# Kernel tuning notes

Hardware: AMD Instinct MI355X
Metric: run time of the kernel (lower is better)

Reference implementation:

```python
import jax, jax.numpy as jnp
import numpy as np

N_HEADS = 16
EMBED = 1024
SEQ = 2048
BATCH = 4
GELU_C = 0.044715
EPS = 1e-5


def gelu_tanh(x):
    return 0.5 * x * (1.0 + jnp.tanh(jnp.sqrt(2.0 / jnp.pi) * (x + GELU_C * x ** 3)))


def layer_norm(x, scale, shift):
    mean = jnp.mean(x, axis=-1, keepdims=True)
    var = jnp.var(x, axis=-1, keepdims=True)
    return scale * (x - mean) / jnp.sqrt(var + EPS) + shift


def setup_inputs() -> dict:
    key = jax.random.key(0)
    ks = jax.random.split(key, 8)
    d = EMBED
    s = 0.02
    return {
        "X": jax.random.normal(ks[0], (BATCH, SEQ, d), dtype=jnp.float32),
        "Wq": jax.random.normal(ks[1], (d, d), dtype=jnp.float32) * s,
        "Wk": jax.random.normal(ks[2], (d, d), dtype=jnp.float32) * s,
        "Wv": jax.random.normal(ks[3], (d, d), dtype=jnp.float32) * s,
        "Wo": jax.random.normal(ks[4], (d, d), dtype=jnp.float32) * s,
        "W1": jax.random.normal(ks[5], (d, 4 * d), dtype=jnp.float32) * s,
        "b1": jnp.zeros((4 * d,), dtype=jnp.float32),
        "W2": jax.random.normal(ks[6], (4 * d, d), dtype=jnp.float32) * s,
        "b2": jnp.zeros((d,), dtype=jnp.float32),
        "ln1_scale": jnp.ones((d,), dtype=jnp.float32),
        "ln1_shift": jnp.zeros((d,), dtype=jnp.float32),
        "ln2_scale": jnp.ones((d,), dtype=jnp.float32),
        "ln2_shift": jnp.zeros((d,), dtype=jnp.float32),
    }


def attention(x, Wq, Wk, Wv, Wo):
    b, s, d = x.shape
    h, dh = N_HEADS, d // N_HEADS
    q = (x @ Wq).reshape(b, s, h, dh).transpose(0, 2, 1, 3)  # [b,h,s,dh]
    k = (x @ Wk).reshape(b, s, h, dh).transpose(0, 2, 1, 3)
    v = (x @ Wv).reshape(b, s, h, dh).transpose(0, 2, 1, 3)
    scores = jnp.einsum("bhqd,bhkd->bhqk", q, k) / jnp.sqrt(jnp.float32(dh))
    causal = jnp.tril(jnp.ones((s, s), dtype=bool))
    scores = jnp.where(causal, scores, -jnp.inf)
    w = jax.nn.softmax(scores, axis=-1)  # dropout rate 0 -> identity
    ctx = jnp.einsum("bhqk,bhkd->bhqd", w, v)
    ctx = ctx.transpose(0, 2, 1, 3).reshape(b, s, d)
    return ctx @ Wo


def reference(X, Wq, Wk, Wv, Wo, W1, b1, W2, b2,
              ln1_scale, ln1_shift, ln2_scale, ln2_shift):
    h = layer_norm(X, ln1_scale, ln1_shift)
    X = X + attention(h, Wq, Wk, Wv, Wo)
    h = layer_norm(X, ln2_scale, ln2_shift)
    h = gelu_tanh(h @ W1 + b1) @ W2 + b2
    return X + h
```

## Files before the change

### kernel.cpp

```cpp
#include <hip/hip_runtime.h>

typedef unsigned short u16;
typedef __attribute__((ext_vector_type(8))) short bf16x8;
typedef __attribute__((ext_vector_type(4))) float fx4;

#define MFMA16(a, b, c) __builtin_amdgcn_mfma_f32_16x16x32_bf16((a), (b), (c), 0, 0, 0)

__device__ __forceinline__ u16 f2bf(float f) {
  unsigned u = __float_as_uint(f);
  u += 0x7fffu + ((u >> 16) & 1u);
  return (u16)(u >> 16);
}

__device__ __forceinline__ void gload_lds16(const void* g, void* l) {
  __builtin_amdgcn_global_load_lds((const __attribute__((address_space(1))) void*)g,
                                   (__attribute__((address_space(3))) void*)l,
                                   16, 0, 0);
}

struct WP {
  const float* s[6];
  u16* d[6];
};
__global__ __launch_bounds__(256) void tcvt_all(WP p) {
  __shared__ float t[32][33];
  const int id = blockIdx.x;
  int which, bx, by, R, C;
  if (id < 4096) {
    which = id >> 10;
    const int q = id & 1023;
    bx = q >> 5; by = q & 31; R = 1024; C = 1024;
  } else if (id < 8192) {
    which = 4;
    const int q = id - 4096;
    bx = q & 127; by = q >> 7; R = 1024; C = 4096;
  } else {
    which = 5;
    const int q = id - 8192;
    bx = q & 31; by = q >> 5; R = 4096; C = 1024;
  }
  const float* src = p.s[which];
  u16* dst = p.d[which];
  const int tx = threadIdx.x & 31, ty = threadIdx.x >> 5;
#pragma unroll
  for (int i = 0; i < 4; ++i)
    t[ty + i * 8][tx] = src[(size_t)(by * 32 + ty + i * 8) * C + bx * 32 + tx];
  __syncthreads();
#pragma unroll
  for (int i = 0; i < 4; ++i)
    dst[(size_t)(bx * 32 + ty + i * 8) * R + by * 32 + tx] = f2bf(t[tx][ty + i * 8]);
}

__global__ __launch_bounds__(256) void ln_kernel(const float* __restrict__ x,
                                                 const float* __restrict__ sc,
                                                 const float* __restrict__ sh,
                                                 u16* __restrict__ out) {
  const int row = blockIdx.x, tid = threadIdx.x;
  const float4 v = ((const float4*)(x + (size_t)row * 1024))[tid];
  float s = v.x + v.y + v.z + v.w;
  float ss = v.x * v.x + v.y * v.y + v.z * v.z + v.w * v.w;
#pragma unroll
  for (int d = 32; d >= 1; d >>= 1) {
    s += __shfl_xor(s, d);
    ss += __shfl_xor(ss, d);
  }
  __shared__ float rs[4], rq[4];
  const int w = tid >> 6;
  if ((tid & 63) == 0) { rs[w] = s; rq[w] = ss; }
  __syncthreads();
  s = rs[0] + rs[1] + rs[2] + rs[3];
  ss = rq[0] + rq[1] + rq[2] + rq[3];
  const float mean = s * (1.f / 1024.f);
  const float var = ss * (1.f / 1024.f) - mean * mean;
  const float rstd = rsqrtf(var + 1e-5f);
  const float4 g = ((const float4*)sc)[tid];
  const float4 b = ((const float4*)sh)[tid];
  ushort4 o;
  o.x = f2bf(g.x * (v.x - mean) * rstd + b.x);
  o.y = f2bf(g.y * (v.y - mean) * rstd + b.y);
  o.z = f2bf(g.z * (v.z - mean) * rstd + b.z);
  o.w = f2bf(g.w * (v.w - mean) * rstd + b.w);
  ((ushort4*)(out + (size_t)row * 1024))[tid] = o;
}

__device__ __forceinline__ void xcd_map(int bid, int NTN, int& tMi, int& tNi) {
  const int xcd = bid & 7, i = bid >> 3;
  tMi = xcd + 8 * (i / NTN);
  tNi = i % NTN;
}

#define EPILOGUE(MODE, MRv)                                                        \
  _Pragma("unroll") for (int m = 0; m < (MRv); ++m) {                              \
    const int rgb = tM + wm * ((MRv) * 16) + m * 16 + hi * 4;                      \
    _Pragma("unroll") for (int n = 0; n < 4; ++n) {                                \
      const int cg = tN + wn * 64 + n * 16 + lo;                                   \
      _Pragma("unroll") for (int r = 0; r < 4; ++r) {                              \
        const float v = acc[m][n][r];                                              \
        const int rg = rgb + r;                                                    \
        if constexpr ((MODE) == 0) {                                               \
          const int which = cg >> 10, c = cg & 1023;                               \
          const int head = c >> 6, dhi = c & 63;                                   \
          const int b = rg >> 11, sidx = rg & 2047;                                \
          const int bh = b * 16 + head;                                            \
          const u16 bv = f2bf(v);                                                  \
          if (which == 0)      qd[((size_t)bh * 2048 + sidx) * 64 + dhi] = bv;     \
          else if (which == 1) kd[((size_t)bh * 2048 + sidx) * 64 + dhi] = bv;     \
          else                 vd[((size_t)bh * 64 + dhi) * 2048 + sidx] = bv;     \
        } else if constexpr ((MODE) == 1) {                                        \
          float* o = (float*)outp;                                                 \
          const size_t idx = (size_t)rg * 1024 + cg;                               \
          o[idx] = aux[idx] + v;                                                   \
        } else if constexpr ((MODE) == 2) {                                        \
          const float xx = v + aux[cg];                                            \
          const float t2 = xx + 0.044715f * xx * xx * xx;                          \
          const float e = __expf(1.5957691216057308f * t2);                        \
          const float th = 1.f - 2.f / (e + 1.f);                                  \
          ((u16*)outp)[(size_t)rg * 4096 + cg] = f2bf(0.5f * xx * (1.f + th));     \
        } else {                                                                   \
          float* o = (float*)outp;                                                 \
          const size_t idx = (size_t)rg * 1024 + cg;                               \
          o[idx] = o[idx] + v + aux[cg];                                           \
        }                                                                          \
      }                                                                            \
    }                                                                              \
  }

template <int MODE>
__global__ __launch_bounds__(512, 1) void gemm4p(
    const u16* __restrict__ A, const u16* __restrict__ Bt, int K, int NTN,
    void* __restrict__ outp, const float* __restrict__ aux,
    u16* __restrict__ qd, u16* __restrict__ kd, u16* __restrict__ vd) {
  __shared__ u16 lA[2][2][256 * 32];
  __shared__ u16 lB[2][2][128 * 32];
  const int tid = threadIdx.x;
  const int lane = tid & 63, w = tid >> 6;
  const int lo = lane & 15, hi = lane >> 4;
  const int wm = w >> 1, wn = w & 1;
  int tMi, tNi;
  xcd_map(blockIdx.x, NTN, tMi, tNi);
  const int tM = tMi * 256, tN = tNi * 128;
  const int NT = K >> 6;
  const int NIT = K >> 7;

#define STG4(TI, H, GK)                                                           \
  do {                                                                            \
    _Pragma("unroll") for (int j = 0; j < 2; ++j) {                               \
      const int idx = j * 512 + tid;                                              \
      const int row = idx >> 2, u = idx & 3;                                      \
      gload_lds16(A + (size_t)(tM + row) * K + (GK) + ((u ^ ((row >> 1) & 3)) * 8), \
                  &lA[TI][H][idx * 8]);                                           \
    }                                                                             \
    {                                                                             \
      const int row = tid >> 2, u = tid & 3;                                      \
      gload_lds16(Bt + (size_t)(tN + row) * K + (GK) + ((u ^ ((row >> 1) & 3)) * 8), \
                  &lB[TI][H][tid * 8]);                                           \
    }                                                                             \
  } while (0)

#define PHASE4(TI, H, STAGE_STMT, VMSTR)                                          \
  {                                                                               \
    bf16x8 afr[4], bfr[4];                                                        \
    _Pragma("unroll") for (int mi = 0; mi < 4; ++mi) {                            \
      const int R = wm * 64 + mi * 16 + lo;                                       \
      afr[mi] = *(const bf16x8*)&lA[TI][H][R * 32 + ((hi ^ ((R >> 1) & 3)) * 8)]; \
    }                                                                             \
    _Pragma("unroll") for (int n = 0; n < 4; ++n) {                               \
      const int R = wn * 64 + n * 16 + lo;                                        \
      bfr[n] = *(const bf16x8*)&lB[TI][H][R * 32 + ((hi ^ ((R >> 1) & 3)) * 8)];  \
    }                                                                             \
    STAGE_STMT;                                                                   \
    asm volatile("s_waitcnt " VMSTR ::: "memory");                                \
    __builtin_amdgcn_s_barrier();                                                 \
    asm volatile("s_waitcnt lgkmcnt(0)" ::: "memory");                            \
    __builtin_amdgcn_sched_barrier(0);                                            \
    __builtin_amdgcn_s_setprio(1);                                                \
    _Pragma("unroll") for (int mi = 0; mi < 4; ++mi)                              \
      _Pragma("unroll") for (int n = 0; n < 4; ++n)                               \
        acc[mi][n] = MFMA16(afr[mi], bfr[n], acc[mi][n]);                         \
    __builtin_amdgcn_s_setprio(0);                                                \
    __builtin_amdgcn_sched_barrier(0);                                            \
    __builtin_amdgcn_s_barrier();                                                 \
    __builtin_amdgcn_sched_barrier(0);                                            \
  }

  fx4 acc[4][4];
#pragma unroll
  for (int m = 0; m < 4; ++m)
#pragma unroll
    for (int n = 0; n < 4; ++n) acc[m][n] = (fx4){0.f, 0.f, 0.f, 0.f};

  STG4(0, 0, 0);
  STG4(0, 1, 32);
  STG4(1, 0, 64);
  asm volatile("s_waitcnt vmcnt(6)" ::: "memory");
  __builtin_amdgcn_s_barrier();
  __builtin_amdgcn_sched_barrier(0);

  for (int it = 0; it < NIT - 1; ++it) {
    const int t0 = 2 * it;
    PHASE4(0, 0, STG4(1, 1, (t0 + 1) * 64 + 32), "vmcnt(6)")
    PHASE4(0, 1, STG4(0, 0, (t0 + 2) * 64), "vmcnt(6)")
    PHASE4(1, 0, STG4(0, 1, (t0 + 2) * 64 + 32), "vmcnt(6)")
    PHASE4(1, 1, STG4(1, 0, (t0 + 3) * 64), "vmcnt(6)")
  }
  {
    const int t0 = NT - 2;
    PHASE4(0, 0, STG4(1, 1, (t0 + 1) * 64 + 32), "vmcnt(6)")
    PHASE4(0, 1, ((void)0), "vmcnt(3)")
    PHASE4(1, 0, ((void)0), "vmcnt(0)")
    PHASE4(1, 1, ((void)0), "vmcnt(0)")
  }
#undef PHASE4
#undef STG4

  EPILOGUE(MODE, 4)
}

template <int MODE>
__global__ __launch_bounds__(512, 1) void gemm8p(
    const u16* __restrict__ A, const u16* __restrict__ Bt, int K, int NTN,
    void* __restrict__ outp, const float* __restrict__ aux,
    u16* __restrict__ qd, u16* __restrict__ kd, u16* __restrict__ vd) {
  constexpr int MR = 8, MR2 = 4;
  __shared__ u16 lA[2][2][256 * 32];
  __shared__ u16 lB[2][2][256 * 32];
  const int tid = threadIdx.x;
  const int lane = tid & 63, w = tid >> 6;
  const int lo = lane & 15, hi = lane >> 4;
  const int wm = w >> 2, wn = w & 3;
  int tMi, tNi;
  xcd_map(blockIdx.x, NTN, tMi, tNi);
  const int tM = tMi * 256, tN = tNi * 256;
  const int NT = K >> 6;
  const int NIT = K >> 7;

#define STG_A(TI, KSH, GK)                                                        \
  do {                                                                            \
    _Pragma("unroll") for (int j = 0; j < 2; ++j) {                               \
      const int idx = j * 512 + tid;                                              \
      const int row = idx >> 2, u = idx & 3;                                      \
      gload_lds16(A + (size_t)(tM + row) * K + (GK) + ((u ^ ((row >> 1) & 3)) * 8), \
                  &lA[TI][KSH][idx * 8]);                                         \
    }                                                                             \
  } while (0)
#define STG_B(TI, KSH, GK)                                                        \
  do {                                                                            \
    _Pragma("unroll") for (int j = 0; j < 2; ++j) {                               \
      const int idx = j * 512 + tid;                                              \
      const int row = idx >> 2, u = idx & 3;                                      \
      gload_lds16(Bt + (size_t)(tN + row) * K + (GK) + ((u ^ ((row >> 1) & 3)) * 8), \
                  &lB[TI][KSH][idx * 8]);                                         \
    }                                                                             \
  } while (0)
#define VMW asm volatile("s_waitcnt vmcnt(4)" ::: "memory")
#define NOPS ((void)0)

#define PHASE(P, STAGE_STMT, VM)                                                  \
  {                                                                               \
    constexpr int ksg = (P) >> 1;                                                 \
    constexpr int mh = (P) & 1;                                                   \
    constexpr int ti = ksg >> 1;                                                  \
    constexpr int ksh = ksg & 1;                                                  \
    bf16x8 afr[MR2];                                                              \
    _Pragma("unroll") for (int mi = 0; mi < MR2; ++mi) {                          \
      const int R = wm * (MR * 16) + (mh * MR2 + mi) * 16 + lo;                   \
      afr[mi] =                                                                   \
          *(const bf16x8*)&lA[ti][ksh][R * 32 + ((hi ^ ((R >> 1) & 3)) * 8)];     \
    }                                                                             \
    if constexpr (mh == 0) {                                                      \
      _Pragma("unroll") for (int n = 0; n < 4; ++n) {                             \
        const int R = wn * 64 + n * 16 + lo;                                      \
        bfr[n] =                                                                  \
            *(const bf16x8*)&lB[ti][ksh][R * 32 + ((hi ^ ((R >> 1) & 3)) * 8)];   \
      }                                                                           \
    }                                                                             \
    STAGE_STMT;                                                                   \
    VM;                                                                           \
    __builtin_amdgcn_s_barrier();                                                 \
    asm volatile("s_waitcnt lgkmcnt(0)" ::: "memory");                            \
    __builtin_amdgcn_sched_barrier(0);                                            \
    __builtin_amdgcn_s_setprio(1);                                                \
    _Pragma("unroll") for (int mi = 0; mi < MR2; ++mi)                            \
      _Pragma("unroll") for (int n = 0; n < 4; ++n)                               \
        acc[mh * MR2 + mi][n] = MFMA16(afr[mi], bfr[n], acc[mh * MR2 + mi][n]);   \
    __builtin_amdgcn_s_setprio(0);                                                \
    __builtin_amdgcn_sched_barrier(0);                                            \
    __builtin_amdgcn_s_barrier();                                                 \
    __builtin_amdgcn_sched_barrier(0);                                            \
  }

  fx4 acc[MR][4];
#pragma unroll
  for (int m = 0; m < MR; ++m)
#pragma unroll
    for (int n = 0; n < 4; ++n) acc[m][n] = (fx4){0.f, 0.f, 0.f, 0.f};
  bf16x8 bfr[4];

  STG_A(0, 0, 0);
  STG_B(0, 0, 0);
  STG_A(0, 1, 32);
  STG_B(0, 1, 32);
  STG_A(1, 0, 64);
  STG_B(1, 0, 64);
  asm volatile("s_waitcnt vmcnt(4)" ::: "memory");
  __builtin_amdgcn_s_barrier();
  __builtin_amdgcn_sched_barrier(0);

  for (int it = 0; it < NIT; ++it) {
    const int t0 = 2 * it;
    const bool g2 = (t0 + 2) < NT, g3 = (t0 + 3) < NT;
    PHASE(0, STG_A(1, 1, (t0 + 1) * 64 + 32), NOPS)
    PHASE(1, STG_B(1, 1, (t0 + 1) * 64 + 32), NOPS)
    PHASE(2, if (g2) STG_A(0, 0, (t0 + 2) * 64), NOPS)
    PHASE(3, if (g2) STG_B(0, 0, (t0 + 2) * 64), VMW)
    PHASE(4, if (g2) STG_A(0, 1, (t0 + 2) * 64 + 32), NOPS)
    PHASE(5, if (g2) STG_B(0, 1, (t0 + 2) * 64 + 32), NOPS)
    PHASE(6, if (g3) STG_A(1, 0, (t0 + 3) * 64), NOPS)
    PHASE(7, if (g3) STG_B(1, 0, (t0 + 3) * 64), VMW)
  }
#undef PHASE
#undef STG_A
#undef STG_B
#undef VMW
#undef NOPS

  EPILOGUE(MODE, MR)
}

__global__ __launch_bounds__(512) void attn_kernel(const u16* __restrict__ Q,
                                                   const u16* __restrict__ Kg,
                                                   const u16* __restrict__ Vt,
                                                   u16* __restrict__ ctx) {
  __shared__ u16 lK[2][64 * 64];
  __shared__ u16 lV[2][64 * 64];
  __shared__ u16 Plds[8][16 * 64];
  const int tid = threadIdx.x;
  const int w = tid >> 6, lane = tid & 63;
  const int lo = lane & 15, hi = lane >> 4;
  const int bh = blockIdx.x;
  const int j = blockIdx.y;
  const u16* Qb = Q + (size_t)bh * 2048 * 64;
  const u16* Kb = Kg + (size_t)bh * 2048 * 64;
  const u16* Vb = Vt + (size_t)bh * 64 * 2048;
  u16* Pw = Plds[w];
  const int nt0 = 2 * j + 2;

  const int rowS = tid >> 3;
  const int ugS = (tid & 7) ^ (rowS & 7);

#define STAGE(BUF, KB)                                                         \
  do {                                                                         \
    gload_lds16(Kb + (size_t)((KB) + rowS) * 64 + ugS * 8, &lK[BUF][tid * 8]); \
    gload_lds16(Vb + (size_t)rowS * 2048 + (KB) + ugS * 8, &lV[BUF][tid * 8]); \
  } while (0)

  const int b = bh >> 4, h = bh & 15;
  const float SCALE = 0.18033688011112042f;

  bf16x8 ones;
#pragma unroll
  for (int i = 0; i < 8; ++i) ones[i] = (short)0x3F80;

  int qt = j;
  int qw = qt * 128 + w * 16;

  bf16x8 qf[2];
#pragma unroll
  for (int kc = 0; kc < 2; ++kc)
    qf[kc] = *(const bf16x8*)&Qb[(size_t)(qw + lo) * 64 + kc * 32 + hi * 8];

  fx4 accO[4];
  fx4 accS = (fx4){0.f, 0.f, 0.f, 0.f};
#pragma unroll
  for (int t2 = 0; t2 < 4; ++t2) accO[t2] = (fx4){0.f, 0.f, 0.f, 0.f};

  STAGE(0, 0);
  __syncthreads();

  int buf = 0;
  for (int t = 0; t < 34; ++t) {
    if (t + 1 < 34) {
      const int tn = t + 1;
      const int kbn = (tn < nt0 ? tn : tn - nt0) * 64;
      STAGE(buf ^ 1, kbn);
    }
    if (t == nt0) {
#pragma unroll
      for (int t2 = 0; t2 < 4; ++t2)
#pragma unroll
        for (int r = 0; r < 4; ++r) {
          const int rg = b * 2048 + qw + hi * 4 + r;
          const int cg = h * 64 + t2 * 16 + lo;
          ctx[(size_t)rg * 1024 + cg] = f2bf(accO[t2][r] / accS[r]);
        }
      qt = 15 - j;
      qw = qt * 128 + w * 16;
#pragma unroll
      for (int kc = 0; kc < 2; ++kc)
        qf[kc] = *(const bf16x8*)&Qb[(size_t)(qw + lo) * 64 + kc * 32 + hi * 8];
#pragma unroll
      for (int t2 = 0; t2 < 4; ++t2) accO[t2] = (fx4){0.f, 0.f, 0.f, 0.f};
      accS = (fx4){0.f, 0.f, 0.f, 0.f};
    }
    const int kb = (t < nt0 ? t : t - nt0) * 64;
    if (kb <= qw + 15) {
      const u16* lKb = lK[buf];
      const u16* lVb = lV[buf];
      fx4 s[4];
#pragma unroll
      for (int tt = 0; tt < 4; ++tt) {
        const int r = tt * 16 + lo;
        const bf16x8 kf0 = *(const bf16x8*)&lKb[r * 64 + ((hi ^ (r & 7)) << 3)];
        const bf16x8 kf1 = *(const bf16x8*)&lKb[r * 64 + (((4 + hi) ^ (r & 7)) << 3)];
        fx4 z = (fx4){0.f, 0.f, 0.f, 0.f};
        z = MFMA16(qf[0], kf0, z);
        z = MFMA16(qf[1], kf1, z);
        s[tt] = z;
      }
      if (kb + 63 > qw) {
#pragma unroll
        for (int tt = 0; tt < 4; ++tt)
#pragma unroll
          for (int r = 0; r < 4; ++r) {
            const int key = kb + tt * 16 + lo;
            const int qr = qw + hi * 4 + r;
            s[tt][r] = (key > qr) ? 0.f : exp2f(s[tt][r] * SCALE);
          }
      } else {
#pragma unroll
        for (int tt = 0; tt < 4; ++tt)
#pragma unroll
          for (int r = 0; r < 4; ++r) s[tt][r] = exp2f(s[tt][r] * SCALE);
      }
#pragma unroll
      for (int r = 0; r < 4; ++r) {
        unsigned pk01, pk23;
        asm("v_cvt_pk_bf16_f32 %0, %1, %2" : "=v"(pk01) : "v"(s[0][r]), "v"(s[1][r]));
        asm("v_cvt_pk_bf16_f32 %0, %1, %2" : "=v"(pk23) : "v"(s[2][r]), "v"(s[3][r]));
        const int row = hi * 4 + r;
        const int sw = (row & 7) << 4;
        const int rbase = row * 128;
        Pw[(rbase + (((0 * 16 + lo) * 2) ^ sw)) >> 1] = (u16)pk01;
        Pw[(rbase + (((1 * 16 + lo) * 2) ^ sw)) >> 1] = (u16)(pk01 >> 16);
        Pw[(rbase + (((2 * 16 + lo) * 2) ^ sw)) >> 1] = (u16)pk23;
        Pw[(rbase + (((3 * 16 + lo) * 2) ^ sw)) >> 1] = (u16)(pk23 >> 16);
      }
      asm volatile("s_waitcnt lgkmcnt(0)" ::: "memory");
      bf16x8 pf[2];
#pragma unroll
      for (int kc = 0; kc < 2; ++kc) {
        const int row = lo;
        const int colB = kc * 64 + hi * 16;
        pf[kc] = *(const bf16x8*)((const char*)Pw + row * 128 + (colB ^ ((row & 7) << 4)));
      }
      accS = MFMA16(pf[0], ones, accS);
      accS = MFMA16(pf[1], ones, accS);
#pragma unroll
      for (int t2 = 0; t2 < 4; ++t2) {
        const int r2 = t2 * 16 + lo;
        const bf16x8 vf0 = *(const bf16x8*)&lVb[r2 * 64 + ((hi ^ (r2 & 7)) << 3)];
        const bf16x8 vf1 = *(const bf16x8*)&lVb[r2 * 64 + (((4 + hi) ^ (r2 & 7)) << 3)];
        accO[t2] = MFMA16(pf[0], vf0, accO[t2]);
        accO[t2] = MFMA16(pf[1], vf1, accO[t2]);
      }
    }
    __syncthreads();
    buf ^= 1;
  }
#pragma unroll
  for (int t2 = 0; t2 < 4; ++t2)
#pragma unroll
    for (int r = 0; r < 4; ++r) {
      const int rg = b * 2048 + qw + hi * 4 + r;
      const int cg = h * 64 + t2 * 16 + lo;
      ctx[(size_t)rg * 1024 + cg] = f2bf(accO[t2][r] / accS[r]);
    }
#undef STAGE
}

extern "C" void kernel_launch(void* const* d_in, const int* in_sizes, int n_in,
                              void* d_out, int out_size, void* d_ws, size_t ws_size,
                              hipStream_t stream) {
  const float* X    = (const float*)d_in[0];
  const float* Wq   = (const float*)d_in[1];
  const float* Wk   = (const float*)d_in[2];
  const float* Wv   = (const float*)d_in[3];
  const float* Wo   = (const float*)d_in[4];
  const float* W1   = (const float*)d_in[5];
  const float* b1   = (const float*)d_in[6];
  const float* W2   = (const float*)d_in[7];
  const float* b2   = (const float*)d_in[8];
  const float* ln1s = (const float*)d_in[9];
  const float* ln1b = (const float*)d_in[10];
  const float* ln2s = (const float*)d_in[11];
  const float* ln2b = (const float*)d_in[12];

  const size_t SZ_WQKVT = 3072UL * 1024;
  const size_t SZ_WOT   = 1024UL * 1024;
  const size_t SZ_W1T   = 4096UL * 1024;
  const size_t SZ_W2T   = 1024UL * 4096;
  const size_t SZ_H     = 8192UL * 1024;
  const size_t SZ_QKV   = 64UL * 2048 * 64;

  u16* WqkvT = (u16*)d_ws;
  u16* WoT   = WqkvT + SZ_WQKVT;
  u16* W1T   = WoT + SZ_WOT;
  u16* W2T   = W1T + SZ_W1T;
  u16* hbuf  = W2T + SZ_W2T;
  u16* qbuf  = hbuf + SZ_H;
  u16* kbuf  = qbuf + SZ_QKV;
  u16* vbuf  = kbuf + SZ_QKV;
  u16* gbuf  = vbuf + SZ_QKV;
  u16* ctx   = hbuf;
  u16* h2    = qbuf;

  float* out = (float*)d_out;
  dim3 blk(256);

  WP wp;
  wp.s[0] = Wq; wp.s[1] = Wk; wp.s[2] = Wv; wp.s[3] = Wo; wp.s[4] = W1; wp.s[5] = W2;
  wp.d[0] = WqkvT;
  wp.d[1] = WqkvT + 1024 * 1024;
  wp.d[2] = WqkvT + 2 * 1024 * 1024;
  wp.d[3] = WoT;
  wp.d[4] = W1T;
  wp.d[5] = W2T;
  tcvt_all<<<12288, blk, 0, stream>>>(wp);

  ln_kernel<<<8192, blk, 0, stream>>>(X, ln1s, ln1b, hbuf);
  gemm4p<0><<<768, dim3(512), 0, stream>>>(hbuf, WqkvT, 1024, 24,
                                           nullptr, nullptr, qbuf, kbuf, vbuf);
  attn_kernel<<<dim3(64, 8), dim3(512), 0, stream>>>(qbuf, kbuf, vbuf, ctx);
  gemm4p<1><<<256, dim3(512), 0, stream>>>(ctx, WoT, 1024, 8,
                                           out, X, nullptr, nullptr, nullptr);
  ln_kernel<<<8192, blk, 0, stream>>>(out, ln2s, ln2b, h2);
  gemm8p<2><<<512, dim3(512), 0, stream>>>(h2, W1T, 1024, 16,
                                           gbuf, b1, nullptr, nullptr, nullptr);
  gemm4p<3><<<256, dim3(512), 0, stream>>>(gbuf, W2T, 4096, 8,
                                           out, b2, nullptr, nullptr, nullptr);
}
```

Measured before the change: 396.5 us.

## Double-buffer LDS fragment registers to overlap ds_reads with MFMAs in GEMMs

Both GEMM kernels (gemm4p-style and gemm8p) now hold two register sets for the A and B fragments. The LDS reads for the next phase are issued right after the barrier, alongside the current phase's MFMA block, instead of before it. The goal is to hide LDS read latency behind matrix math. This costs more VGPRs, and the lgkmcnt(0) wait at the next phase may still stall. In gemm8p the mid-loop vmcnt waits also change from every fourth phase to every phase, and the loop gains a peeled tail.

```diff
diff --git a/kernel.cpp b/kernel.cpp
--- a/kernel.cpp
+++ b/kernel.cpp
@@ -157,26 +157,30 @@
     }                                                                             \
   } while (0)
 
-#define PHASE4(TI, H, STAGE_STMT, VMSTR)                                          \
-  {                                                                               \
-    bf16x8 afr[4], bfr[4];                                                        \
+#define LDFRAG4(AF, BF, TI, H)                                                    \
+  do {                                                                            \
     _Pragma("unroll") for (int mi = 0; mi < 4; ++mi) {                            \
       const int R = wm * 64 + mi * 16 + lo;                                       \
-      afr[mi] = *(const bf16x8*)&lA[TI][H][R * 32 + ((hi ^ ((R >> 1) & 3)) * 8)]; \
+      AF[mi] = *(const bf16x8*)&lA[TI][H][R * 32 + ((hi ^ ((R >> 1) & 3)) * 8)];  \
     }                                                                             \
     _Pragma("unroll") for (int n = 0; n < 4; ++n) {                               \
       const int R = wn * 64 + n * 16 + lo;                                        \
-      bfr[n] = *(const bf16x8*)&lB[TI][H][R * 32 + ((hi ^ ((R >> 1) & 3)) * 8)];  \
-    }                                                                             \
+      BF[n] = *(const bf16x8*)&lB[TI][H][R * 32 + ((hi ^ ((R >> 1) & 3)) * 8)];   \
+    }                                                                             \
+  } while (0)
+
+#define PHASE4(CA, CB, PREF_STMT, STAGE_STMT, VMSTR)                              \
+  {                                                                               \
     STAGE_STMT;                                                                   \
     asm volatile("s_waitcnt " VMSTR ::: "memory");                                \
     __builtin_amdgcn_s_barrier();                                                 \
     asm volatile("s_waitcnt lgkmcnt(0)" ::: "memory");                            \
     __builtin_amdgcn_sched_barrier(0);                                            \
+    PREF_STMT;                                                                    \
     __builtin_amdgcn_s_setprio(1);                                                \
     _Pragma("unroll") for (int mi = 0; mi < 4; ++mi)                              \
       _Pragma("unroll") for (int n = 0; n < 4; ++n)                               \
-        acc[mi][n] = MFMA16(afr[mi], bfr[n], acc[mi][n]);                         \
+        acc[mi][n] = MFMA16(CA[mi], CB[n], acc[mi][n]);                           \
     __builtin_amdgcn_s_setprio(0);                                                \
     __builtin_amdgcn_sched_barrier(0);                                            \
     __builtin_amdgcn_s_barrier();                                                 \
@@ -188,6 +192,7 @@
   for (int m = 0; m < 4; ++m)
 #pragma unroll
     for (int n = 0; n < 4; ++n) acc[m][n] = (fx4){0.f, 0.f, 0.f, 0.f};
+  bf16x8 afrA[4], bfrA[4], afrB[4], bfrB[4];
 
   STG4(0, 0, 0);
   STG4(0, 1, 32);
@@ -195,22 +200,24 @@
   asm volatile("s_waitcnt vmcnt(6)" ::: "memory");
   __builtin_amdgcn_s_barrier();
   __builtin_amdgcn_sched_barrier(0);
+  LDFRAG4(afrA, bfrA, 0, 0);
 
   for (int it = 0; it < NIT - 1; ++it) {
     const int t0 = 2 * it;
-    PHASE4(0, 0, STG4(1, 1, (t0 + 1) * 64 + 32), "vmcnt(6)")
-    PHASE4(0, 1, STG4(0, 0, (t0 + 2) * 64), "vmcnt(6)")
-    PHASE4(1, 0, STG4(0, 1, (t0 + 2) * 64 + 32), "vmcnt(6)")
-    PHASE4(1, 1, STG4(1, 0, (t0 + 3) * 64), "vmcnt(6)")
+    PHASE4(afrA, bfrA, LDFRAG4(afrB, bfrB, 0, 1), STG4(1, 1, (t0 + 1) * 64 + 32), "vmcnt(6)")
+    PHASE4(afrB, bfrB, LDFRAG4(afrA, bfrA, 1, 0), STG4(0, 0, (t0 + 2) * 64), "vmcnt(6)")
+    PHASE4(afrA, bfrA, LDFRAG4(afrB, bfrB, 1, 1), STG4(0, 1, (t0 + 2) * 64 + 32), "vmcnt(6)")
+    PHASE4(afrB, bfrB, LDFRAG4(afrA, bfrA, 0, 0), STG4(1, 0, (t0 + 3) * 64), "vmcnt(6)")
   }
   {
     const int t0 = NT - 2;
-    PHASE4(0, 0, STG4(1, 1, (t0 + 1) * 64 + 32), "vmcnt(6)")
-    PHASE4(0, 1, ((void)0), "vmcnt(3)")
-    PHASE4(1, 0, ((void)0), "vmcnt(0)")
-    PHASE4(1, 1, ((void)0), "vmcnt(0)")
+    PHASE4(afrA, bfrA, LDFRAG4(afrB, bfrB, 0, 1), STG4(1, 1, (t0 + 1) * 64 + 32), "vmcnt(6)")
+    PHASE4(afrB, bfrB, LDFRAG4(afrA, bfrA, 1, 0), ((void)0), "vmcnt(3)")
+    PHASE4(afrA, bfrA, LDFRAG4(afrB, bfrB, 1, 1), ((void)0), "vmcnt(0)")
+    PHASE4(afrB, bfrB, ((void)0), ((void)0), "vmcnt(0)")
   }
 #undef PHASE4
+#undef LDFRAG4
 #undef STG4
 
   EPILOGUE(MODE, 4)
@@ -221,7 +228,6 @@
     const u16* __restrict__ A, const u16* __restrict__ Bt, int K, int NTN,
     void* __restrict__ outp, const float* __restrict__ aux,
     u16* __restrict__ qd, u16* __restrict__ kd, u16* __restrict__ vd) {
-  constexpr int MR = 8, MR2 = 4;
   __shared__ u16 lA[2][2][256 * 32];
   __shared__ u16 lB[2][2][256 * 32];
   const int tid = threadIdx.x;
@@ -231,7 +237,6 @@
   int tMi, tNi;
   xcd_map(blockIdx.x, NTN, tMi, tNi);
   const int tM = tMi * 256, tN = tNi * 256;
-  const int NT = K >> 6;
   const int NIT = K >> 7;
 
 #define STG_A(TI, KSH, GK)                                                        \
@@ -252,49 +257,46 @@
                   &lB[TI][KSH][idx * 8]);                                         \
     }                                                                             \
   } while (0)
-#define VMW asm volatile("s_waitcnt vmcnt(4)" ::: "memory")
-#define NOPS ((void)0)
-
-#define PHASE(P, STAGE_STMT, VM)                                                  \
+
+#define LDA8(AF, TI, KSH, MH)                                                     \
+  do {                                                                            \
+    _Pragma("unroll") for (int mi = 0; mi < 4; ++mi) {                            \
+      const int R = wm * 128 + ((MH) * 4 + mi) * 16 + lo;                         \
+      AF[mi] = *(const bf16x8*)&lA[TI][KSH][R * 32 + ((hi ^ ((R >> 1) & 3)) * 8)]; \
+    }                                                                             \
+  } while (0)
+#define LDB8(BF, TI, KSH)                                                         \
+  do {                                                                            \
+    _Pragma("unroll") for (int n = 0; n < 4; ++n) {                               \
+      const int R = wn * 64 + n * 16 + lo;                                        \
+      BF[n] = *(const bf16x8*)&lB[TI][KSH][R * 32 + ((hi ^ ((R >> 1) & 3)) * 8)]; \
+    }                                                                             \
+  } while (0)
+
+#define PHASE8(MH, CA, CB, PREF_STMT, STAGE_STMT, VMSTR)                          \
   {                                                                               \
-    constexpr int ksg = (P) >> 1;                                                 \
-    constexpr int mh = (P) & 1;                                                   \
-    constexpr int ti = ksg >> 1;                                                  \
-    constexpr int ksh = ksg & 1;                                                  \
-    bf16x8 afr[MR2];                                                              \
-    _Pragma("unroll") for (int mi = 0; mi < MR2; ++mi) {                          \
-      const int R = wm * (MR * 16) + (mh * MR2 + mi) * 16 + lo;                   \
-      afr[mi] =                                                                   \
-          *(const bf16x8*)&lA[ti][ksh][R * 32 + ((hi ^ ((R >> 1) & 3)) * 8)];     \
-    }                                                                             \
-    if constexpr (mh == 0) {                                                      \
-      _Pragma("unroll") for (int n = 0; n < 4; ++n) {                             \
-        const int R = wn * 64 + n * 16 + lo;                                      \
-        bfr[n] =                                                                  \
-            *(const bf16x8*)&lB[ti][ksh][R * 32 + ((hi ^ ((R >> 1) & 3)) * 8)];   \
-      }                                                                           \
-    }                                                                             \
     STAGE_STMT;                                                                   \
-    VM;                                                                           \
+    asm volatile("s_waitcnt " VMSTR ::: "memory");                                \
     __builtin_amdgcn_s_barrier();                                                 \
     asm volatile("s_waitcnt lgkmcnt(0)" ::: "memory");                            \
     __builtin_amdgcn_sched_barrier(0);                                            \
+    PREF_STMT;                                                                    \
     __builtin_amdgcn_s_setprio(1);                                                \
-    _Pragma("unroll") for (int mi = 0; mi < MR2; ++mi)                            \
+    _Pragma("unroll") for (int mi = 0; mi < 4; ++mi)                              \
       _Pragma("unroll") for (int n = 0; n < 4; ++n)                               \
-        acc[mh * MR2 + mi][n] = MFMA16(afr[mi], bfr[n], acc[mh * MR2 + mi][n]);   \
+        acc[(MH) * 4 + mi][n] = MFMA16(CA[mi], CB[n], acc[(MH) * 4 + mi][n]);     \
     __builtin_amdgcn_s_setprio(0);                                                \
     __builtin_amdgcn_sched_barrier(0);                                            \
     __builtin_amdgcn_s_barrier();                                                 \
     __builtin_amdgcn_sched_barrier(0);                                            \
   }
 
-  fx4 acc[MR][4];
-#pragma unroll
-  for (int m = 0; m < MR; ++m)
+  fx4 acc[8][4];
+#pragma unroll
+  for (int m = 0; m < 8; ++m)
 #pragma unroll
     for (int n = 0; n < 4; ++n) acc[m][n] = (fx4){0.f, 0.f, 0.f, 0.f};
-  bf16x8 bfr[4];
+  bf16x8 afrA[4], afrB[4], bfrA[4], bfrB[4];
 
   STG_A(0, 0, 0);
   STG_B(0, 0, 0);
@@ -305,26 +307,38 @@
   asm volatile("s_waitcnt vmcnt(4)" ::: "memory");
   __builtin_amdgcn_s_barrier();
   __builtin_amdgcn_sched_barrier(0);
-
-  for (int it = 0; it < NIT; ++it) {
+  LDA8(afrA, 0, 0, 0);
+  LDB8(bfrA, 0, 0);
+
+  for (int it = 0; it < NIT - 1; ++it) {
     const int t0 = 2 * it;
-    const bool g2 = (t0 + 2) < NT, g3 = (t0 + 3) < NT;
-    PHASE(0, STG_A(1, 1, (t0 + 1) * 64 + 32), NOPS)
-    PHASE(1, STG_B(1, 1, (t0 + 1) * 64 + 32), NOPS)
-    PHASE(2, if (g2) STG_A(0, 0, (t0 + 2) * 64), NOPS)
-    PHASE(3, if (g2) STG_B(0, 0, (t0 + 2) * 64), VMW)
-    PHASE(4, if (g2) STG_A(0, 1, (t0 + 2) * 64 + 32), NOPS)
-    PHASE(5, if (g2) STG_B(0, 1, (t0 + 2) * 64 + 32), NOPS)
-    PHASE(6, if (g3) STG_A(1, 0, (t0 + 3) * 64), NOPS)
-    PHASE(7, if (g3) STG_B(1, 0, (t0 + 3) * 64), VMW)
-  }
-#undef PHASE
+    PHASE8(0, afrA, bfrA, LDA8(afrB, 0, 0, 1), STG_A(1, 1, (t0 + 1) * 64 + 32), "vmcnt(4)")
+    PHASE8(1, afrB, bfrA, { LDA8(afrA, 0, 1, 0); LDB8(bfrB, 0, 1); }, STG_B(1, 1, (t0 + 1) * 64 + 32), "vmcnt(4)")
+    PHASE8(0, afrA, bfrB, LDA8(afrB, 0, 1, 1), STG_A(0, 0, (t0 + 2) * 64), "vmcnt(4)")
+    PHASE8(1, afrB, bfrB, { LDA8(afrA, 1, 0, 0); LDB8(bfrA, 1, 0); }, STG_B(0, 0, (t0 + 2) * 64), "vmcnt(4)")
+    PHASE8(0, afrA, bfrA, LDA8(afrB, 1, 0, 1), STG_A(0, 1, (t0 + 2) * 64 + 32), "vmcnt(4)")
+    PHASE8(1, afrB, bfrA, { LDA8(afrA, 1, 1, 0); LDB8(bfrB, 1, 1); }, STG_B(0, 1, (t0 + 2) * 64 + 32), "vmcnt(4)")
+    PHASE8(0, afrA, bfrB, LDA8(afrB, 1, 1, 1), STG_A(1, 0, (t0 + 3) * 64), "vmcnt(4)")
+    PHASE8(1, afrB, bfrB, { LDA8(afrA, 0, 0, 0); LDB8(bfrA, 0, 0); }, STG_B(1, 0, (t0 + 3) * 64), "vmcnt(4)")
+  }
+  {
+    const int t0 = 2 * (NIT - 1);
+    PHASE8(0, afrA, bfrA, LDA8(afrB, 0, 0, 1), STG_A(1, 1, (t0 + 1) * 64 + 32), "vmcnt(4)")
+    PHASE8(1, afrB, bfrA, { LDA8(afrA, 0, 1, 0); LDB8(bfrB, 0, 1); }, STG_B(1, 1, (t0 + 1) * 64 + 32), "vmcnt(4)")
+    PHASE8(0, afrA, bfrB, LDA8(afrB, 0, 1, 1), ((void)0), "vmcnt(4)")
+    PHASE8(1, afrB, bfrB, { LDA8(afrA, 1, 0, 0); LDB8(bfrA, 1, 0); }, ((void)0), "vmcnt(4)")
+    PHASE8(0, afrA, bfrA, LDA8(afrB, 1, 0, 1), ((void)0), "vmcnt(0)")
+    PHASE8(1, afrB, bfrA, { LDA8(afrA, 1, 1, 0); LDB8(bfrB, 1, 1); }, ((void)0), "vmcnt(0)")
+    PHASE8(0, afrA, bfrB, LDA8(afrB, 1, 1, 1), ((void)0), "vmcnt(0)")
+    PHASE8(1, afrB, bfrB, ((void)0), ((void)0), "vmcnt(0)")
+  }
+#undef PHASE8
+#undef LDA8
+#undef LDB8
 #undef STG_A
 #undef STG_B
-#undef VMW
-#undef NOPS
-
-  EPILOGUE(MODE, MR)
+
+  EPILOGUE(MODE, 8)
 }
 
 __global__ __launch_bounds__(512) void attn_kernel(const u16* __restrict__ Q,
```

New measurement: 417.5 us. 5.3% more time.
